# Optimization experiments

Measured on AMD Instinct MI355X. Metric: run time of the kernel, lower is better.

## Reference

```python
import jax, jax.numpy as jnp
import numpy as np

NUM_HEADS = 16
HEAD_DIM = 128  # embedding_size 2048 / 16 heads
ROPE_BASE = 10000.0


def rope_tables(seq_len, head_dim):
    # matches precompute_rope_params with freq_config=None
    inv_freq = 1.0 / (ROPE_BASE ** (jnp.arange(0, head_dim, 2, dtype=jnp.float32) / head_dim))
    pos = jnp.arange(seq_len, dtype=jnp.float32)
    ang = pos[:, None] * inv_freq[None, :]          # [S, D/2]
    ang = jnp.concatenate([ang, ang], axis=1)        # [S, D]
    return jnp.cos(ang), jnp.sin(ang)


def apply_rope(x, cos, sin):
    # x: [B, H, S, D]
    d = x.shape[-1]
    x1, x2 = x[..., : d // 2], x[..., d // 2:]
    rotated = jnp.concatenate([-x2, x1], axis=-1)
    return x * cos[None, None] + rotated * sin[None, None]


def setup_inputs() -> dict:
    key = jax.random.key(0)
    ks = jax.random.split(key, 5)
    B, S, H = 2, 2048, 2048
    w_scale = 1.0 / np.sqrt(H)  # keep activations sane
    return {
        "x": jax.random.normal(ks[0], (B, S, H), dtype=jnp.float32),
        "Wq": jax.random.normal(ks[1], (H, H), dtype=jnp.float32) * w_scale,
        "Wk": jax.random.normal(ks[2], (H, H), dtype=jnp.float32) * w_scale,
        "Wv": jax.random.normal(ks[3], (H, H), dtype=jnp.float32) * w_scale,
        "Wo": jax.random.normal(ks[4], (H, H), dtype=jnp.float32) * w_scale,
    }


def reference(x, Wq, Wk, Wv, Wo):
    B, S, H = x.shape
    nH, D = NUM_HEADS, HEAD_DIM
    # torch Linear(bias=False): y = x @ W.T
    q = (x @ Wq.T).reshape(B, S, nH, D).transpose(0, 2, 1, 3)  # [B,H,S,D]
    k = (x @ Wk.T).reshape(B, S, nH, D).transpose(0, 2, 1, 3)
    v = (x @ Wv.T).reshape(B, S, nH, D).transpose(0, 2, 1, 3)
    cos, sin = rope_tables(S, D)
    q = apply_rope(q, cos, sin)
    k = apply_rope(k, cos, sin)  # note: v is NOT rotated, matching source
    # Faithful to source bug: scores / (1/sqrt(d)) == scores * sqrt(d)
    scale = jnp.sqrt(jnp.asarray(D, dtype=x.dtype))
    scores = jnp.einsum("bhqd,bhkd->bhqk", q, k) * scale
    causal = jnp.triu(jnp.ones((S, S), dtype=bool), k=1)
    scores = jnp.where(causal[None, None], -jnp.inf, scores)
    attn = jax.nn.softmax(scores, axis=-1)
    ctx = jnp.einsum("bhqk,bhkd->bhqd", attn, v)
    ctx = ctx.transpose(0, 2, 1, 3).reshape(B, S, H)
    return ctx @ Wo.T
```

## Files before the change

### kernel.cpp

```cpp
#include <hip/hip_runtime.h>
#include <cmath>


typedef unsigned short u16;
typedef __attribute__((ext_vector_type(4))) float  f32x4;
typedef __attribute__((ext_vector_type(16))) float f32x16;
typedef __attribute__((ext_vector_type(4))) float  float4v;
typedef __attribute__((ext_vector_type(4))) unsigned short u16x4;
typedef __attribute__((ext_vector_type(8))) unsigned short u16x8;
typedef __attribute__((ext_vector_type(8))) short s16x8;

__device__ __forceinline__ u16 f2bf(float f) {
  unsigned u = __float_as_uint(f);
  u += 0x7FFFu + ((u >> 16) & 1u);
  return (u16)(u >> 16);
}
__device__ __forceinline__ float bf2f(u16 h) {
  return __uint_as_float(((unsigned)h) << 16);
}
__device__ __forceinline__ f32x16 MFMA32(s16x8 a, s16x8 b, f32x16 c) {
  return __builtin_amdgcn_mfma_f32_32x32x16_bf16(a, b, c, 0, 0, 0);
}
__device__ __forceinline__ unsigned cvtpk_bf16(float lo, float hi) {
  unsigned r;
  asm("v_cvt_pk_bf16_f32 %0, %1, %2" : "=v"(r) : "v"(lo), "v"(hi));
  return r;
}
__device__ __forceinline__ void gld16(const void* g, void* s) {
  __builtin_amdgcn_global_load_lds(
      (const __attribute__((address_space(1))) void*)g,
      (__attribute__((address_space(3))) void*)s, 16, 0, 0);
}

__global__ void split_bf16(const float* __restrict__ src, u16* __restrict__ hi,
                           u16* __restrict__ lo, int n4) {
  int i = blockIdx.x * 256 + threadIdx.x;
  if (i >= n4) return;
  float4v v = ((const float4v*)src)[i];
  u16x4 hv, lv;
#pragma unroll
  for (int j = 0; j < 4; ++j) {
    float f = v[j];
    u16 h = f2bf(f);
    hv[j] = h;
    lv[j] = f2bf(f - bf2f(h));
  }
  ((u16x4*)hi)[i] = hv;
  if (lo) ((u16x4*)lo)[i] = lv;
}

__global__ void rope_tab(float* __restrict__ cosT, float* __restrict__ sinT) {
  int idx = blockIdx.x * 256 + threadIdx.x;
  int i = idx & 63, s = idx >> 6;
  double invf = pow(10000.0, -(double)i / 64.0);
  double ang = (double)s * invf;
  cosT[idx] = (float)cos(ang);
  sinT[idx] = (float)sin(ang);
}

__global__ __launch_bounds__(512, 2)
void gemm_qk(const u16* __restrict__ xh, const u16* __restrict__ xl,
             const u16* __restrict__ Wqh, const u16* __restrict__ Wql,
             const u16* __restrict__ Wkh, const u16* __restrict__ Wkl,
             u16* __restrict__ Qh, u16* __restrict__ Ql,
             u16* __restrict__ Kh, u16* __restrict__ Kl,
             const float* __restrict__ cosT, const float* __restrict__ sinT,
             float qscale, int M, int N, int K) {
  __shared__ u16 SM[2 * 32768];
  const int t = threadIdx.x;
  const int w = t >> 6, lane = t & 63;
  const int l31 = lane & 31, hi = lane >> 5;
  const int wm = w >> 1, wn = w & 1;

  const int bid = (int)blockIdx.x + 16 * (int)blockIdx.y;
  const int xcd = bid & 7, slot = bid >> 3;
  const int bn = 2 * xcd + (slot & 1);
  const int bm = slot >> 1;

  const size_t arow0 = (size_t)bm * 256, brow0 = (size_t)bn * 128;

  const int pA0 = 128 * w + lane;
  const int pA1 = pA0 + 64;
  const int pB0 = 64 * w + lane;
  const int qA0 = pA0 ^ ((pA0 >> 3) & 7);
  const int qA1 = pA1 ^ ((pA1 >> 3) & 7);
  const int qB0 = pB0 ^ ((pB0 >> 3) & 7);
  const size_t gA0 = (arow0 + (qA0 >> 2)) * (size_t)K + (qA0 & 3) * 8;
  const size_t gA1 = (arow0 + (qA1 >> 2)) * (size_t)K + (qA1 & 3) * 8;
  const size_t gB0 = (brow0 + (qB0 >> 2)) * (size_t)K + (qB0 & 3) * 8;

  auto stage = [&](int k0, int bp) {
    u16* P = &SM[bp * 32768];
    gld16(&xh[gA0 + k0], P + 1024 * w);
    gld16(&xh[gA1 + k0], P + 1024 * w + 512);
    gld16(&xl[gA0 + k0], P + 8192 + 1024 * w);
    gld16(&xl[gA1 + k0], P + 8192 + 1024 * w + 512);
    gld16(&Wqh[gB0 + k0], P + 16384 + 512 * w);
    gld16(&Wql[gB0 + k0], P + 20480 + 512 * w);
    gld16(&Wkh[gB0 + k0], P + 24576 + 512 * w);
    gld16(&Wkl[gB0 + k0], P + 28672 + 512 * w);
  };

  auto aoff = [&](int fm, int ks) {
    int q = ((64 * wm + 32 * fm + l31) << 2) | (2 * ks + hi);
    q ^= (q >> 3) & 7;
    return q * 8;
  };
  auto boff = [&](int fn, int ks) {
    int q = ((32 * wn + 64 * fn + l31) << 2) | (2 * ks + hi);
    q ^= (q >> 3) & 7;
    return q * 8;
  };

  f32x16 accq[2][2], acck[2][2];
#pragma unroll
  for (int fm = 0; fm < 2; ++fm)
#pragma unroll
    for (int fn = 0; fn < 2; ++fn)
#pragma unroll
      for (int r = 0; r < 16; ++r) { accq[fm][fn][r] = 0.f; acck[fm][fn][r] = 0.f; }

  const int NK = K >> 5;
  stage(0, 0);
  int bp = 0;
  for (int kt = 0; kt < NK; ++kt) {
    if (kt + 1 < NK) {
      stage((kt + 1) * 32, bp ^ 1);
      asm volatile("s_waitcnt vmcnt(8)" ::: "memory");
    } else {
      asm volatile("s_waitcnt vmcnt(0)" ::: "memory");
    }
    __builtin_amdgcn_sched_barrier(0);
    __builtin_amdgcn_s_barrier();
    __builtin_amdgcn_sched_barrier(0);

    const u16* P = &SM[bp * 32768];
#pragma unroll
    for (int ks = 0; ks < 2; ++ks) {
      s16x8 a_h[2], a_l[2], b_h[2], b_l[2];
#pragma unroll
      for (int fm = 0; fm < 2; ++fm) {
        a_h[fm] = *(const s16x8*)&P[aoff(fm, ks)];
        a_l[fm] = *(const s16x8*)&P[8192 + aoff(fm, ks)];
      }
#pragma unroll
      for (int fn = 0; fn < 2; ++fn) {
        b_h[fn] = *(const s16x8*)&P[16384 + boff(fn, ks)];
        b_l[fn] = *(const s16x8*)&P[20480 + boff(fn, ks)];
      }
      __builtin_amdgcn_sched_barrier(0);
      __builtin_amdgcn_s_barrier();
      asm volatile("s_waitcnt lgkmcnt(0)" ::: "memory");
      __builtin_amdgcn_sched_barrier(0);
      __builtin_amdgcn_s_setprio(1);
#pragma unroll
      for (int fm = 0; fm < 2; ++fm)
#pragma unroll
        for (int fn = 0; fn < 2; ++fn) {
          accq[fm][fn] = MFMA32(a_h[fm], b_h[fn], accq[fm][fn]);
          accq[fm][fn] = MFMA32(a_h[fm], b_l[fn], accq[fm][fn]);
          accq[fm][fn] = MFMA32(a_l[fm], b_h[fn], accq[fm][fn]);
        }
      __builtin_amdgcn_s_setprio(0);
      __builtin_amdgcn_sched_barrier(0);
      __builtin_amdgcn_s_barrier();
#pragma unroll
      for (int fn = 0; fn < 2; ++fn) {
        b_h[fn] = *(const s16x8*)&P[24576 + boff(fn, ks)];
        b_l[fn] = *(const s16x8*)&P[28672 + boff(fn, ks)];
      }
      __builtin_amdgcn_sched_barrier(0);
      __builtin_amdgcn_s_barrier();
      asm volatile("s_waitcnt lgkmcnt(0)" ::: "memory");
      __builtin_amdgcn_sched_barrier(0);
      __builtin_amdgcn_s_setprio(1);
#pragma unroll
      for (int fm = 0; fm < 2; ++fm)
#pragma unroll
        for (int fn = 0; fn < 2; ++fn) {
          acck[fm][fn] = MFMA32(a_h[fm], b_h[fn], acck[fm][fn]);
          acck[fm][fn] = MFMA32(a_h[fm], b_l[fn], acck[fm][fn]);
          acck[fm][fn] = MFMA32(a_l[fm], b_h[fn], acck[fm][fn]);
        }
      __builtin_amdgcn_s_setprio(0);
      __builtin_amdgcn_sched_barrier(0);
      __builtin_amdgcn_s_barrier();
    }
    bp ^= 1;
  }

  const int hd = 32 * wn + l31;
#pragma unroll
  for (int fm = 0; fm < 2; ++fm)
#pragma unroll
    for (int r = 0; r < 16; ++r) {
      const int row = bm * 256 + 64 * wm + 32 * fm + (r & 3) + 8 * (r >> 2) + 4 * hi;
      const int s = row & 2047;
      const float cs = cosT[s * 64 + hd], sn = sinT[s * 64 + hd];
      const size_t p1 = (size_t)row * N + bn * 128 + hd;
      {
        const float q1 = accq[fm][0][r], q2 = accq[fm][1][r];
        const float o1 = (q1 * cs - q2 * sn) * qscale;
        const float o2 = (q2 * cs + q1 * sn) * qscale;
        const u16 h1 = f2bf(o1);
        Qh[p1] = h1; Ql[p1] = f2bf(o1 - bf2f(h1));
        const u16 h2 = f2bf(o2);
        Qh[p1 + 64] = h2; Ql[p1 + 64] = f2bf(o2 - bf2f(h2));
      }
      {
        const float k1 = acck[fm][0][r], k2 = acck[fm][1][r];
        const float o1 = k1 * cs - k2 * sn;
        const float o2 = k2 * cs + k1 * sn;
        const u16 h1 = f2bf(o1);
        Kh[p1] = h1; Kl[p1] = f2bf(o1 - bf2f(h1));
        const u16 h2 = f2bf(o2);
        Kh[p1 + 64] = h2; Kl[p1 + 64] = f2bf(o2 - bf2f(h2));
      }
    }
}

template <int NTERM, int OMODE, int ROPE, int GX>
__global__ __launch_bounds__(512, NTERM == 3 ? 1 : 4)
void gemm8(const u16* __restrict__ Ah, const u16* __restrict__ Al,
           const u16* __restrict__ Bh, const u16* __restrict__ Bl,
           float* __restrict__ Cf, u16* __restrict__ Ch, u16* __restrict__ Cl,
           const float* __restrict__ cosT, const float* __restrict__ sinT,
           float scale, int M, int N, int K) {
  constexpr int BUF = (NTERM == 3) ? 24576 : 12288;
  constexpr int BHI = (NTERM == 3) ? 16384 : 8192;
  constexpr int PER = GX / 8;
  constexpr int PSH = (PER == 2) ? 1 : 2;
  static_assert(PER == 2 || PER == 4, "grid.x must be 16 or 32");
  __shared__ u16 SM[3 * BUF];
  const int t = threadIdx.x;
  const int w = t >> 6, lane = t & 63;
  const int l31 = lane & 31, hi = lane >> 5;
  const int wm = w >> 1, wn = w & 1;

  const int bid = (int)blockIdx.x + GX * (int)blockIdx.y;
  const int xcd = bid & 7, slot = bid >> 3;
  const int bn = PER * xcd + (slot & (PER - 1));
  const int bm = slot >> PSH;

  const size_t arow0 = (size_t)bm * 256, brow0 = (size_t)bn * 128;

  const int pA0 = 128 * w + lane;
  const int pA1 = pA0 + 64;
  const int pB0 = 64 * w + lane;
  const int qA0 = pA0 ^ ((pA0 >> 3) & 7);
  const int qA1 = pA1 ^ ((pA1 >> 3) & 7);
  const int qB0 = pB0 ^ ((pB0 >> 3) & 7);
  const size_t gA0 = (arow0 + (qA0 >> 2)) * (size_t)K + (qA0 & 3) * 8;
  const size_t gA1 = (arow0 + (qA1 >> 2)) * (size_t)K + (qA1 & 3) * 8;
  const size_t gB0 = (brow0 + (qB0 >> 2)) * (size_t)K + (qB0 & 3) * 8;

  auto stage = [&](int k0, int bp) {
    u16* P = &SM[bp * BUF];
    gld16(&Ah[gA0 + k0], P + 1024 * w);
    gld16(&Ah[gA1 + k0], P + 1024 * w + 512);
    gld16(&Bh[gB0 + k0], P + BHI + 512 * w);
    if constexpr (NTERM == 3) {
      gld16(&Al[gA0 + k0], P + 8192 + 1024 * w);
      gld16(&Al[gA1 + k0], P + 8192 + 1024 * w + 512);
      gld16(&Bl[gB0 + k0], P + BHI + 4096 + 512 * w);
    }
  };

  auto aoff = [&](int fm, int ks) {
    int q = ((64 * wm + 32 * fm + l31) << 2) | (2 * ks + hi);
    q ^= (q >> 3) & 7;
    return q * 8;
  };
  auto boff = [&](int fn, int ks) {
    int q = ((32 * wn + 64 * fn + l31) << 2) | (2 * ks + hi);
    q ^= (q >> 3) & 7;
    return q * 8;
  };

  f32x16 acc[2][2];
#pragma unroll
  for (int fm = 0; fm < 2; ++fm)
#pragma unroll
    for (int fn = 0; fn < 2; ++fn)
#pragma unroll
      for (int r = 0; r < 16; ++r) acc[fm][fn][r] = 0.f;

  const int NK = K >> 5;
  stage(0, 0);
  if (NK > 1) stage(32, 1);
  int cur = 0, nxt = 1, fut = 2;
  for (int kt = 0; kt < NK; ++kt) {
    if (kt + 2 < NK) {
      stage((kt + 2) * 32, fut);
      if constexpr (NTERM == 3)
        asm volatile("s_waitcnt vmcnt(12)" ::: "memory");
      else
        asm volatile("s_waitcnt vmcnt(6)" ::: "memory");
    } else if (kt + 1 < NK) {
      if constexpr (NTERM == 3)
        asm volatile("s_waitcnt vmcnt(6)" ::: "memory");
      else
        asm volatile("s_waitcnt vmcnt(3)" ::: "memory");
    } else {
      asm volatile("s_waitcnt vmcnt(0)" ::: "memory");
    }
    __builtin_amdgcn_sched_barrier(0);
    __builtin_amdgcn_s_barrier();
    __builtin_amdgcn_sched_barrier(0);

    const u16* P = &SM[cur * BUF];
    __builtin_amdgcn_s_setprio(1);
#pragma unroll
    for (int ks = 0; ks < 2; ++ks) {
      s16x8 a_h[2], a_l[2], b_h[2], b_l[2];
#pragma unroll
      for (int fm = 0; fm < 2; ++fm) {
        a_h[fm] = *(const s16x8*)&P[aoff(fm, ks)];
        if constexpr (NTERM == 3)
          a_l[fm] = *(const s16x8*)&P[8192 + aoff(fm, ks)];
      }
#pragma unroll
      for (int fn = 0; fn < 2; ++fn) {
        b_h[fn] = *(const s16x8*)&P[BHI + boff(fn, ks)];
        if constexpr (NTERM == 3)
          b_l[fn] = *(const s16x8*)&P[BHI + 4096 + boff(fn, ks)];
      }
#pragma unroll
      for (int fm = 0; fm < 2; ++fm)
#pragma unroll
        for (int fn = 0; fn < 2; ++fn) {
          acc[fm][fn] = MFMA32(a_h[fm], b_h[fn], acc[fm][fn]);
          if constexpr (NTERM == 3) {
            acc[fm][fn] = MFMA32(a_h[fm], b_l[fn], acc[fm][fn]);
            acc[fm][fn] = MFMA32(a_l[fm], b_h[fn], acc[fm][fn]);
          }
        }
    }
    __builtin_amdgcn_s_setprio(0);
    __builtin_amdgcn_s_barrier();
    const int tmp = cur; cur = nxt; nxt = fut; fut = tmp;
  }

  if constexpr (ROPE) {
    const int hd = 32 * wn + l31;
#pragma unroll
    for (int fm = 0; fm < 2; ++fm)
#pragma unroll
      for (int r = 0; r < 16; ++r) {
        const int row = bm * 256 + 64 * wm + 32 * fm + (r & 3) + 8 * (r >> 2) + 4 * hi;
        const int s = row & 2047;
        const float cs = cosT[s * 64 + hd], sn = sinT[s * 64 + hd];
        const float q1 = acc[fm][0][r], q2 = acc[fm][1][r];
        const float o1 = (q1 * cs - q2 * sn) * scale;
        const float o2 = (q2 * cs + q1 * sn) * scale;
        const size_t p1 = (size_t)row * N + bn * 128 + hd;
        const u16 h1 = f2bf(o1);
        Ch[p1] = h1; Cl[p1] = f2bf(o1 - bf2f(h1));
        const u16 h2 = f2bf(o2);
        Ch[p1 + 64] = h2; Cl[p1 + 64] = f2bf(o2 - bf2f(h2));
      }
  } else {
#pragma unroll
    for (int fm = 0; fm < 2; ++fm)
#pragma unroll
      for (int fn = 0; fn < 2; ++fn)
#pragma unroll
        for (int r = 0; r < 16; ++r) {
          const int row = bm * 256 + 64 * wm + 32 * fm + (r & 3) + 8 * (r >> 2) + 4 * hi;
          const int col = bn * 128 + 32 * wn + 64 * fn + l31;
          const float v = acc[fm][fn][r];
          if constexpr (OMODE == 0) {
            Cf[(size_t)row * N + col] = v;
          } else if constexpr (OMODE == 1) {
            const u16 hv = f2bf(v);
            Ch[(size_t)row * N + col] = hv;
            Cl[(size_t)row * N + col] = f2bf(v - bf2f(hv));
          } else {
            Ch[(size_t)row * N + col] = f2bf(v);
          }
        }
  }
}

__global__ __launch_bounds__(512, 2)
void attn(const u16* __restrict__ Qh, const u16* __restrict__ Ql,
          const u16* __restrict__ Kh, const u16* __restrict__ Kl,
          const u16* __restrict__ Vt, u16* __restrict__ Ctx) {
  __shared__ u16 SMEM[65536];

  const int t = threadIdx.x;
  const int w = t >> 6, lane = t & 63;
  const int l31 = lane & 31, hi = lane >> 5;
  const int swz = (l31 & 7) << 3;
  const int j = w >> 1, kh = w & 1;

  const int bid = (int)blockIdx.x + 8 * (int)blockIdx.y + 128 * (int)blockIdx.z;
  const int xcd = bid & 7, slot = bid >> 3;
  const int h = xcd * 2 + (slot >> 4);
  const int rem = slot & 15;
  const int qtA = rem & 7, bA = rem >> 3;

  const int offK0 = (8 * w + (lane >> 4)) * 2048 + (((lane & 15) ^ ((lane >> 4) & 7)) * 8);
  const int offK1 = (8 * w + 4 + (lane >> 4)) * 2048 + (((lane & 15) ^ ((4 + (lane >> 4)) & 7)) * 8);
  const int offV0 = (16 * w + (lane >> 3)) * 4096 + (((lane & 7) ^ ((lane >> 3) & 7)) * 8);
  const int offV1 = offV0 + 8 * 4096;

  auto stage = [&](const u16* gK, const u16* gKlo, const u16* gV, int kt, int bp) {
    u16* B = &SMEM[bp * 24576];
    const int ka = kt * 131072;
    const int va = kt * 64;
    gld16(gK + ka + offK0, B + 1024 * w);
    gld16(gK + ka + offK1, B + 1024 * w + 512);
    gld16(gKlo + ka + offK0, B + 8192 + 1024 * w);
    gld16(gKlo + ka + offK1, B + 8192 + 1024 * w + 512);
    gld16(gV + va + offV0, B + 16384 + 1024 * w);
    gld16(gV + va + offV1, B + 16384 + 1024 * w + 512);
  };

  int bufph = 0;
  {
    const u16* gK0 = Kh + ((size_t)(bA * 2048)) * 2048 + h * 128;
    const u16* gL0 = Kl + ((size_t)(bA * 2048)) * 2048 + h * 128;
    const u16* gV0 = Vt + (size_t)(h * 128) * 4096 + bA * 2048;
    stage(gK0, gL0, gV0, 0, 0);
  }

  for (int task = 0; task < 2; ++task) {
    const int qt = task ? 15 - qtA : qtA;
    const int bb = task ? 1 - bA : bA;
    const u16* gK0 = Kh + ((size_t)(bb * 2048)) * 2048 + h * 128;
    const u16* gL0 = Kl + ((size_t)(bb * 2048)) * 2048 + h * 128;
    const u16* gV0 = Vt + (size_t)(h * 128) * 4096 + bb * 2048;
    const int nb = 1 - bb;
    const u16* nK0 = Kh + ((size_t)(nb * 2048)) * 2048 + h * 128;
    const u16* nL0 = Kl + ((size_t)(nb * 2048)) * 2048 + h * 128;
    const u16* nV0 = Vt + (size_t)(h * 128) * 4096 + nb * 2048;

    const int q0 = qt * 128 + 32 * j;
    const int qg = q0 + l31;
    s16x8 qfh[8], qfl[8];
    {
      const size_t qbase = ((size_t)(bb * 2048 + qg)) * 2048 + h * 128 + 8 * hi;
#pragma unroll
      for (int s = 0; s < 8; ++s) {
        qfh[s] = *(const s16x8*)&Qh[qbase + 16 * s];
        qfl[s] = *(const s16x8*)&Ql[qbase + 16 * s];
      }
    }

    float m_run = -3.0e38f, l_run = 0.f;
    f32x16 o[4];
#pragma unroll
    for (int d = 0; d < 4; ++d)
#pragma unroll
      for (int r = 0; r < 16; ++r) o[d][r] = 0.f;

    const int nt = 2 * qt + 2;
    for (int kt = 0; kt < nt; ++kt) {
      bool staged = true;
      if (kt + 1 < nt)      stage(gK0, gL0, gV0, kt + 1, bufph ^ 1);
      else if (task == 0)   stage(nK0, nL0, nV0, 0, bufph ^ 1);
      else                  staged = false;
      if (staged) asm volatile("s_waitcnt vmcnt(6)" ::: "memory");
      else        asm volatile("s_waitcnt vmcnt(0)" ::: "memory");
      __builtin_amdgcn_sched_barrier(0);
      __builtin_amdgcn_s_barrier();
      __builtin_amdgcn_sched_barrier(0);

      const int kb0 = kt * 64 + 32 * kh;
      const bool active = (q0 + 31) >= kb0;
      if (active) {
        const u16* Kb = &SMEM[bufph * 24576];
        const u16* Lb = Kb + 8192;
        const u16* Vb = Kb + 16384;
        f32x16 acc;
#pragma unroll
        for (int r = 0; r < 16; ++r) acc[r] = 0.f;
        __builtin_amdgcn_s_setprio(1);
#pragma unroll
        for (int s = 0; s < 8; ++s) {
          const int col = 16 * s + 8 * hi;
          const s16x8 kha = *(const s16x8*)&Kb[((32 * kh + l31) * 128 + col) ^ swz];
          const s16x8 kla = *(const s16x8*)&Lb[((32 * kh + l31) * 128 + col) ^ swz];
          acc = MFMA32(kha, qfh[s], acc);
          acc = MFMA32(kla, qfh[s], acc);
          acc = MFMA32(kha, qfl[s], acc);
        }
        __builtin_amdgcn_s_setprio(0);

        const bool partial = (kb0 + 31) > q0;
        float mx = -3.0e38f;
#pragma unroll
        for (int r = 0; r < 16; ++r) {
          const int koff = (r & 3) + 8 * (r >> 2) + 4 * hi;
          float v = acc[r];
          if (partial && (kb0 + koff > qg)) v = -3.0e38f;
          acc[r] = v;
          mx = fmaxf(mx, v);
        }
        mx = fmaxf(mx, __shfl_xor(mx, 32));
        const float mn = fmaxf(m_run, mx);
        const float al = __expf(m_run - mn);
        m_run = mn;
        float rs = 0.f;
#pragma unroll
        for (int r = 0; r < 16; ++r) {
          const float e = __expf(acc[r] - mn);
          acc[r] = e;
          rs += e;
        }
        rs += __shfl_xor(rs, 32);
        l_run = l_run * al + rs;
#pragma unroll
        for (int d = 0; d < 4; ++d)
#pragma unroll
          for (int r = 0; r < 16; ++r) o[d][r] *= al;

        s16x8 pb[2];
#pragma unroll
        for (int tt = 0; tt < 2; ++tt) {
          const int q2A = 2 * tt;
          const float e0 = acc[4 * q2A + 0], e1 = acc[4 * q2A + 1];
          const float e2 = acc[4 * q2A + 2], e3 = acc[4 * q2A + 3];
          const float f0 = acc[4 * q2A + 4], f1 = acc[4 * q2A + 5];
          const float f2 = acc[4 * q2A + 6], f3 = acc[4 * q2A + 7];
          unsigned a0 = cvtpk_bf16(e0, e1);
          unsigned a1 = cvtpk_bf16(e2, e3);
          unsigned b0 = cvtpk_bf16(f0, f1);
          unsigned b1 = cvtpk_bf16(f2, f3);
          asm volatile("v_permlane32_swap_b32 %0, %1" : "+v"(a0), "+v"(b0));
          asm volatile("v_permlane32_swap_b32 %0, %1" : "+v"(a1), "+v"(b1));
          union { unsigned u[4]; s16x8 v; } pk;
          pk.u[0] = a0; pk.u[1] = a1; pk.u[2] = b0; pk.u[3] = b1;
          pb[tt] = pk.v;
        }

        __builtin_amdgcn_s_setprio(1);
#pragma unroll
        for (int d = 0; d < 4; ++d) {
#pragma unroll
          for (int tt = 0; tt < 2; ++tt) {
            const s16x8 va = *(const s16x8*)
                &Vb[((32 * d + l31) * 64 + 16 * (2 * kh + tt) + 8 * hi) ^ swz];
            o[d] = MFMA32(va, pb[tt], o[d]);
          }
        }
        __builtin_amdgcn_s_setprio(0);
      }
      __builtin_amdgcn_s_barrier();
      bufph ^= 1;
    }

    float* Sf = (float*)&SMEM[49152];
    Sf[w * 64 + lane] = m_run;
    Sf[512 + w * 64 + lane] = l_run;
    asm volatile("s_waitcnt lgkmcnt(0)" ::: "memory");
    __builtin_amdgcn_s_barrier();
    const float mOth = Sf[(w ^ 1) * 64 + lane];
    const float lOth = Sf[512 + (w ^ 1) * 64 + lane];
    const float mC = fmaxf(m_run, mOth);
    const float eS = __expf(m_run - mC);
    const float eO = __expf(mOth - mC);
    const float lC = eS * l_run + eO * lOth;
#pragma unroll
    for (int d = 0; d < 4; ++d)
#pragma unroll
      for (int r = 0; r < 16; ++r) o[d][r] *= eS;
    __builtin_amdgcn_s_barrier();
#pragma unroll
    for (int round = 0; round < 2; ++round) {
      if ((w >> 2) == round && kh == 1) {
        const int sl = j & 1;
#pragma unroll
        for (int d = 0; d < 4; ++d)
#pragma unroll
          for (int rr = 0; rr < 4; ++rr) {
            float4v c;
            c[0] = o[d][4 * rr + 0]; c[1] = o[d][4 * rr + 1];
            c[2] = o[d][4 * rr + 2]; c[3] = o[d][4 * rr + 3];
            const int cidx = 4 * (d * 4 + rr);
            *(float4v*)&Sf[sl * 4096 + ((lane * 64 + cidx) ^ ((lane & 7) << 2))] = c;
          }
      }
      asm volatile("s_waitcnt lgkmcnt(0)" ::: "memory");
      __builtin_amdgcn_s_barrier();
      if ((w >> 2) == round && kh == 0) {
        const int sl = j & 1;
#pragma unroll
        for (int d = 0; d < 4; ++d)
#pragma unroll
          for (int rr = 0; rr < 4; ++rr) {
            const int cidx = 4 * (d * 4 + rr);
            const float4v c =
                *(const float4v*)&Sf[sl * 4096 + ((lane * 64 + cidx) ^ ((lane & 7) << 2))];
            o[d][4 * rr + 0] += c[0]; o[d][4 * rr + 1] += c[1];
            o[d][4 * rr + 2] += c[2]; o[d][4 * rr + 3] += c[3];
          }
      }
      __builtin_amdgcn_s_barrier();
    }
    u16* Os = &SMEM[49152];
    if (kh == 0) {
      const float inv_l = 1.0f / lC;
      const int rl = 32 * j + l31;
#pragma unroll
      for (int d = 0; d < 4; ++d)
#pragma unroll
        for (int r = 0; r < 16; r += 2) {
          const int dd = 32 * d + (r & 3) + 8 * (r >> 2) + 4 * hi;
          const unsigned pr = cvtpk_bf16(o[d][r] * inv_l, o[d][r + 1] * inv_l);
          *(unsigned*)&Os[(rl * 128 + dd) ^ ((rl & 7) << 3)] = pr;
        }
    }
    asm volatile("s_waitcnt lgkmcnt(0)" ::: "memory");
    __builtin_amdgcn_s_barrier();
    {
      const int rr = t >> 2, cb = (t & 3) * 32;
      const size_t ob =
          ((size_t)(bb * 2048 + qt * 128 + rr)) * 2048 + h * 128 + cb;
#pragma unroll
      for (int p = 0; p < 4; ++p)
        *(u16x8*)&Ctx[ob + 8 * p] =
            *(const u16x8*)&Os[(rr * 128 + cb + 8 * p) ^ ((rr & 7) << 3)];
    }
    asm volatile("s_waitcnt lgkmcnt(0)" ::: "memory");
    __builtin_amdgcn_s_barrier();
  }
}

extern "C" void kernel_launch(void* const* d_in, const int* in_sizes, int n_in,
                              void* d_out, int out_size, void* d_ws, size_t ws_size,
                              hipStream_t stream) {
  const float* x  = (const float*)d_in[0];
  const float* Wq = (const float*)d_in[1];
  const float* Wk = (const float*)d_in[2];
  const float* Wv = (const float*)d_in[3];
  const float* Wo = (const float*)d_in[4];
  float* out = (float*)d_out;

  char* ws = (char*)d_ws;
  size_t off = 0;
  auto alloc = [&](size_t bytes) {
    char* p = ws + off;
    off += (bytes + 255) & ~(size_t)255;
    return p;
  };
  const size_t XE = (size_t)4096 * 2048;
  const size_t WE = (size_t)2048 * 2048;

  u16* xh  = (u16*)alloc(XE * 2);
  u16* xl  = (u16*)alloc(XE * 2);
  u16* Wqh = (u16*)alloc(WE * 2);
  u16* Wql = (u16*)alloc(WE * 2);
  u16* Wkh = (u16*)alloc(WE * 2);
  u16* Wkl = (u16*)alloc(WE * 2);
  u16* Wvh = (u16*)alloc(WE * 2);
  u16* Woh = (u16*)alloc(WE * 2);
  u16* Qhb = (u16*)alloc(XE * 2);
  u16* Qlb = (u16*)alloc(XE * 2);
  u16* Khb = (u16*)alloc(XE * 2);
  u16* Klb = (u16*)alloc(XE * 2);
  u16* Vtb = (u16*)alloc(XE * 2);
  u16* Ctxb = (u16*)alloc(XE * 2);
  float* cosT = (float*)alloc((size_t)2048 * 64 * 4);
  float* sinT = (float*)alloc((size_t)2048 * 64 * 4);
  (void)ws_size;
  (void)in_sizes; (void)n_in; (void)out_size;

  split_bf16<<<8192, 256, 0, stream>>>(x, xh, xl, (int)(XE / 4));
  split_bf16<<<4096, 256, 0, stream>>>(Wq, Wqh, Wql, (int)(WE / 4));
  split_bf16<<<4096, 256, 0, stream>>>(Wk, Wkh, Wkl, (int)(WE / 4));
  split_bf16<<<4096, 256, 0, stream>>>(Wv, Wvh, nullptr, (int)(WE / 4));
  split_bf16<<<4096, 256, 0, stream>>>(Wo, Woh, nullptr, (int)(WE / 4));
  rope_tab<<<512, 256, 0, stream>>>(cosT, sinT);

  gemm_qk<<<dim3(16, 16), 512, 0, stream>>>(
      xh, xl, Wqh, Wql, Wkh, Wkl, Qhb, Qlb, Khb, Klb, cosT, sinT,
      11.313708498984760f, 4096, 2048, 2048);
  gemm8<1, 2, 0, 32><<<dim3(32, 8), 512, 0, stream>>>(
      Wvh, nullptr, xh, nullptr, nullptr, Vtb, nullptr, nullptr, nullptr,
      1.0f, 2048, 4096, 2048);

  attn<<<dim3(8, 16, 2), 512, 0, stream>>>(Qhb, Qlb, Khb, Klb, Vtb, Ctxb);

  gemm8<1, 0, 0, 16><<<dim3(16, 16), 512, 0, stream>>>(
      Ctxb, nullptr, Woh, nullptr, out, nullptr, nullptr, nullptr, nullptr,
      1.0f, 4096, 2048, 2048);
}
```

Before: 528.9 us.

## Restructure QK GEMM mainloop to interleave split prefetch stages with MFMA phases

The QK projection GEMM mainloop now loads fragments for both k-substeps at once. It also splits the next-tile global prefetch into an A part, issued before the Q MFMA phase, and a B part, issued before the K MFMA phase. A full vmcnt(0) wait and a barrier at the end of each iteration replace the vmcnt(8) wait at the top. Launch bounds drop from 2 to 1 blocks per CU, giving the kernel more registers for the larger fragment arrays at the cost of occupancy. The aim is to spread global loads across the compute phases and cut barrier count, but ending each iteration on a full memory wait may expose load latency.

```diff
diff --git a/kernel.cpp b/kernel.cpp
--- a/kernel.cpp
+++ b/kernel.cpp
@@ -58,7 +58,7 @@
   sinT[idx] = (float)sin(ang);
 }
 
-__global__ __launch_bounds__(512, 2)
+__global__ __launch_bounds__(512, 1)
 void gemm_qk(const u16* __restrict__ xh, const u16* __restrict__ xl,
              const u16* __restrict__ Wqh, const u16* __restrict__ Wql,
              const u16* __restrict__ Wkh, const u16* __restrict__ Wkl,
@@ -89,12 +89,15 @@
   const size_t gA1 = (arow0 + (qA1 >> 2)) * (size_t)K + (qA1 & 3) * 8;
   const size_t gB0 = (brow0 + (qB0 >> 2)) * (size_t)K + (qB0 & 3) * 8;
 
-  auto stage = [&](int k0, int bp) {
+  auto stageA = [&](int k0, int bp) {
     u16* P = &SM[bp * 32768];
     gld16(&xh[gA0 + k0], P + 1024 * w);
     gld16(&xh[gA1 + k0], P + 1024 * w + 512);
     gld16(&xl[gA0 + k0], P + 8192 + 1024 * w);
     gld16(&xl[gA1 + k0], P + 8192 + 1024 * w + 512);
+  };
+  auto stageB = [&](int k0, int bp) {
+    u16* P = &SM[bp * 32768];
     gld16(&Wqh[gB0 + k0], P + 16384 + 512 * w);
     gld16(&Wql[gB0 + k0], P + 20480 + 512 * w);
     gld16(&Wkh[gB0 + k0], P + 24576 + 512 * w);
@@ -121,70 +124,87 @@
       for (int r = 0; r < 16; ++r) { accq[fm][fn][r] = 0.f; acck[fm][fn][r] = 0.f; }
 
   const int NK = K >> 5;
-  stage(0, 0);
+  stageA(0, 0);
+  stageB(0, 0);
+  asm volatile("s_waitcnt vmcnt(0)" ::: "memory");
+  __builtin_amdgcn_sched_barrier(0);
+  __builtin_amdgcn_s_barrier();
+  __builtin_amdgcn_sched_barrier(0);
+
   int bp = 0;
   for (int kt = 0; kt < NK; ++kt) {
-    if (kt + 1 < NK) {
-      stage((kt + 1) * 32, bp ^ 1);
-      asm volatile("s_waitcnt vmcnt(8)" ::: "memory");
-    } else {
-      asm volatile("s_waitcnt vmcnt(0)" ::: "memory");
-    }
-    __builtin_amdgcn_sched_barrier(0);
-    __builtin_amdgcn_s_barrier();
-    __builtin_amdgcn_sched_barrier(0);
-
     const u16* P = &SM[bp * 32768];
-#pragma unroll
-    for (int ks = 0; ks < 2; ++ks) {
-      s16x8 a_h[2], a_l[2], b_h[2], b_l[2];
-#pragma unroll
-      for (int fm = 0; fm < 2; ++fm) {
-        a_h[fm] = *(const s16x8*)&P[aoff(fm, ks)];
-        a_l[fm] = *(const s16x8*)&P[8192 + aoff(fm, ks)];
-      }
-#pragma unroll
-      for (int fn = 0; fn < 2; ++fn) {
-        b_h[fn] = *(const s16x8*)&P[16384 + boff(fn, ks)];
-        b_l[fn] = *(const s16x8*)&P[20480 + boff(fn, ks)];
-      }
+    const bool more = (kt + 1 < NK);
+
+    s16x8 a_h[2][2], a_l[2][2];
+    {
+      s16x8 bq_h[2][2], bq_l[2][2];
+#pragma unroll
+      for (int ks = 0; ks < 2; ++ks)
+#pragma unroll
+        for (int fm = 0; fm < 2; ++fm) {
+          a_h[ks][fm] = *(const s16x8*)&P[aoff(fm, ks)];
+          a_l[ks][fm] = *(const s16x8*)&P[8192 + aoff(fm, ks)];
+        }
+#pragma unroll
+      for (int ks = 0; ks < 2; ++ks)
+#pragma unroll
+        for (int fn = 0; fn < 2; ++fn) {
+          bq_h[ks][fn] = *(const s16x8*)&P[16384 + boff(fn, ks)];
+          bq_l[ks][fn] = *(const s16x8*)&P[20480 + boff(fn, ks)];
+        }
+      if (more) stageA((kt + 1) * 32, bp ^ 1);
       __builtin_amdgcn_sched_barrier(0);
       __builtin_amdgcn_s_barrier();
       asm volatile("s_waitcnt lgkmcnt(0)" ::: "memory");
       __builtin_amdgcn_sched_barrier(0);
       __builtin_amdgcn_s_setprio(1);
 #pragma unroll
-      for (int fm = 0; fm < 2; ++fm)
+      for (int ks = 0; ks < 2; ++ks)
+#pragma unroll
+        for (int fm = 0; fm < 2; ++fm)
+#pragma unroll
+          for (int fn = 0; fn < 2; ++fn) {
+            accq[fm][fn] = MFMA32(a_h[ks][fm], bq_h[ks][fn], accq[fm][fn]);
+            accq[fm][fn] = MFMA32(a_h[ks][fm], bq_l[ks][fn], accq[fm][fn]);
+            accq[fm][fn] = MFMA32(a_l[ks][fm], bq_h[ks][fn], accq[fm][fn]);
+          }
+      __builtin_amdgcn_s_setprio(0);
+      __builtin_amdgcn_sched_barrier(0);
+      __builtin_amdgcn_s_barrier();
+      __builtin_amdgcn_sched_barrier(0);
+    }
+
+    {
+      s16x8 bk_h[2][2], bk_l[2][2];
+#pragma unroll
+      for (int ks = 0; ks < 2; ++ks)
 #pragma unroll
         for (int fn = 0; fn < 2; ++fn) {
-          accq[fm][fn] = MFMA32(a_h[fm], b_h[fn], accq[fm][fn]);
-          accq[fm][fn] = MFMA32(a_h[fm], b_l[fn], accq[fm][fn]);
-          accq[fm][fn] = MFMA32(a_l[fm], b_h[fn], accq[fm][fn]);
-        }
-      __builtin_amdgcn_s_setprio(0);
-      __builtin_amdgcn_sched_barrier(0);
-      __builtin_amdgcn_s_barrier();
-#pragma unroll
-      for (int fn = 0; fn < 2; ++fn) {
-        b_h[fn] = *(const s16x8*)&P[24576 + boff(fn, ks)];
-        b_l[fn] = *(const s16x8*)&P[28672 + boff(fn, ks)];
-      }
+          bk_h[ks][fn] = *(const s16x8*)&P[24576 + boff(fn, ks)];
+          bk_l[ks][fn] = *(const s16x8*)&P[28672 + boff(fn, ks)];
+        }
+      if (more) stageB((kt + 1) * 32, bp ^ 1);
       __builtin_amdgcn_sched_barrier(0);
       __builtin_amdgcn_s_barrier();
       asm volatile("s_waitcnt lgkmcnt(0)" ::: "memory");
       __builtin_amdgcn_sched_barrier(0);
       __builtin_amdgcn_s_setprio(1);
 #pragma unroll
-      for (int fm = 0; fm < 2; ++fm)
-#pragma unroll
-        for (int fn = 0; fn < 2; ++fn) {
-          acck[fm][fn] = MFMA32(a_h[fm], b_h[fn], acck[fm][fn]);
-          acck[fm][fn] = MFMA32(a_h[fm], b_l[fn], acck[fm][fn]);
-          acck[fm][fn] = MFMA32(a_l[fm], b_h[fn], acck[fm][fn]);
-        }
+      for (int ks = 0; ks < 2; ++ks)
+#pragma unroll
+        for (int fm = 0; fm < 2; ++fm)
+#pragma unroll
+          for (int fn = 0; fn < 2; ++fn) {
+            acck[fm][fn] = MFMA32(a_h[ks][fm], bk_h[ks][fn], acck[fm][fn]);
+            acck[fm][fn] = MFMA32(a_h[ks][fm], bk_l[ks][fn], acck[fm][fn]);
+            acck[fm][fn] = MFMA32(a_l[ks][fm], bk_h[ks][fn], acck[fm][fn]);
+          }
       __builtin_amdgcn_s_setprio(0);
       __builtin_amdgcn_sched_barrier(0);
+      asm volatile("s_waitcnt vmcnt(0)" ::: "memory");
       __builtin_amdgcn_s_barrier();
+      __builtin_amdgcn_sched_barrier(0);
     }
     bp ^= 1;
   }
```

New measurement: 519.8 us. Within noise of the previous version (-1.7%).
